# Optimization experiments

Measured on AMD Instinct MI355X. Metric: run time of the kernel, lower is better.

Reference implementation:

```python
import jax, jax.numpy as jnp
import numpy as np

NUM_EXPERTS = 8
PHM_DIM = 4


def setup_inputs() -> dict:
    key = jax.random.key(0)
    k1, k2, k3, k4 = jax.random.split(key, 4)
    bsz, seq, D, O, E, p = 4, 2048, 2048, 2048, NUM_EXPERTS, PHM_DIM
    hidden_states = jax.random.normal(k1, (bsz, seq, D), dtype=jnp.float32)
    gate_w = jax.random.normal(k2, (D, E), dtype=jnp.float32) * 0.02
    phm_rule = jax.random.normal(k3, (E, p, p, p), dtype=jnp.float32) * 0.1
    W = jax.random.normal(k4, (E, p, D // p, O // p), dtype=jnp.float32) * 0.02
    b = jnp.zeros((E, O), dtype=jnp.float32)
    return {"hidden_states": hidden_states, "gate_w": gate_w,
            "phm_rule": phm_rule, "W": W, "b": b}


def reference(hidden_states, gate_w, phm_rule, W, b):
    bsz, seq, dim = hidden_states.shape
    E = gate_w.shape[1]
    x = hidden_states.reshape(-1, dim)                      # [T, D]
    logits = x @ gate_w                                     # [T, E]
    prob = jax.nn.softmax(logits, axis=-1)                  # [T, E]
    gate = jnp.argmax(prob, axis=-1)                        # [T]
    # load-balancing loss
    num_tokens = jnp.sum(jax.nn.one_hot(gate, E, dtype=jnp.int32), axis=0)  # [E]
    f = num_tokens.astype(prob.dtype)
    f = f / jnp.sum(f)
    P = jnp.mean(prob, axis=0)
    balance_loss = E * jnp.sum(P * f)
    # PHM weight per expert: H_e = sum_p kron(phm_rule[e,p], W[e,p]) -> [E, D, O]
    Wfull = jnp.einsum('epab,epij->eaibj', phm_rule, W).reshape(E, dim, -1)
    # dense evaluation of every expert on every token, then top-1 select
    all_out = jnp.einsum('td,edo->teo', x, Wfull) + b[None, :, :]  # [T, E, O]
    tok_prob = jnp.take_along_axis(prob, gate[:, None], axis=1)    # [T, 1]
    out = jnp.take_along_axis(all_out, gate[:, None, None], axis=1)[:, 0, :] * tok_prob
    out = out.reshape(bsz, seq, -1)
    return out, balance_loss, num_tokens
```

## Files before the change

kernel.cpp:

```cpp
#include <hip/hip_runtime.h>
#include <cstdint>
#include <cstddef>

typedef _Float16 f16;
typedef f16 f16x2 __attribute__((ext_vector_type(2)));
typedef f16 f16x4 __attribute__((ext_vector_type(4)));
typedef f16 f16x8 __attribute__((ext_vector_type(8)));
typedef float f32x4 __attribute__((ext_vector_type(4)));

#define NEXP 8
#define BM 128
#define BN 128
#define BK 32

__device__ __forceinline__ void async_cp16(void* lds, const void* gsrc) {
  __builtin_amdgcn_global_load_lds(
      (const __attribute__((address_space(1))) void*)gsrc,
      (__attribute__((address_space(3))) void*)lds, 16, 0, 0);
}

__global__ __launch_bounds__(256) void k_gate(
    const float* __restrict__ x, const float* __restrict__ gw,
    f16* __restrict__ xb, int* __restrict__ gate, float* __restrict__ scale,
    int* __restrict__ cnt, float* __restrict__ probsum, int D)
{
  __shared__ float ps[NEXP];
  __shared__ int pc[NEXP];
  int tid = threadIdx.x, lane = tid & 63, w = tid >> 6;
  if (tid < NEXP) { ps[tid] = 0.f; pc[tid] = 0; }
  __syncthreads();

  int t = blockIdx.x * 4 + w;
  const float* xr = x + (size_t)t * D;
  f16* xbr = xb + (size_t)t * D;

  float acc[NEXP] = {};
  for (int d0 = lane * 4; d0 < D; d0 += 256) {
    float4 v = *(const float4*)(xr + d0);
    f16x4 h; h[0] = (f16)v.x; h[1] = (f16)v.y; h[2] = (f16)v.z; h[3] = (f16)v.w;
    *(f16x4*)(xbr + d0) = h;
    const float* g0 = gw + (size_t)d0 * NEXP;
    float xv[4] = {v.x, v.y, v.z, v.w};
#pragma unroll
    for (int j = 0; j < 4; j++) {
      float4 ga = *(const float4*)(g0 + j * NEXP);
      float4 gb = *(const float4*)(g0 + j * NEXP + 4);
      acc[0] += xv[j] * ga.x; acc[1] += xv[j] * ga.y;
      acc[2] += xv[j] * ga.z; acc[3] += xv[j] * ga.w;
      acc[4] += xv[j] * gb.x; acc[5] += xv[j] * gb.y;
      acc[6] += xv[j] * gb.z; acc[7] += xv[j] * gb.w;
    }
  }
#pragma unroll
  for (int e = 0; e < NEXP; e++) {
    float v = acc[e];
    for (int o = 32; o > 0; o >>= 1) v += __shfl_xor(v, o);
    acc[e] = v;
  }
  if (lane == 0) {
    float m = acc[0]; int g = 0;
#pragma unroll
    for (int e = 1; e < NEXP; e++) if (acc[e] > m) { m = acc[e]; g = e; }
    float pr[NEXP]; float ssum = 0.f;
#pragma unroll
    for (int e = 0; e < NEXP; e++) { pr[e] = expf(acc[e] - m); ssum += pr[e]; }
    float inv = 1.0f / ssum;
#pragma unroll
    for (int e = 0; e < NEXP; e++) atomicAdd(&ps[e], pr[e] * inv);
    atomicAdd(&pc[g], 1);
    gate[t] = g;
    scale[t] = pr[g] * inv;
  }
  __syncthreads();
  if (tid < NEXP) {
    atomicAdd(&probsum[tid], ps[tid]);
    atomicAdd(&cnt[tid], pc[tid]);
  }
}

__global__ __launch_bounds__(256) void k_wfull(
    const float* __restrict__ Wp, const float* __restrict__ rule,
    f16* __restrict__ wt, int Dp, int Op, int D, int O)
{
  int bid = blockIdx.x;
  int it = Dp >> 5, jt = Op >> 5;
  int itile = bid % it; bid /= it;
  int jtile = bid % jt; bid /= jt;
  int b = bid & 3; bid >>= 2;
  int e = bid;
  int i0 = itile * 32, j0 = jtile * 32;

  __shared__ float Wt[4][32][33];
  int tid = threadIdx.x;
  for (int idx = tid; idx < 4096; idx += 256) {
    int p = idx >> 10, rem = idx & 1023, ii = rem >> 5, jj = rem & 31;
    Wt[p][ii][jj] = Wp[(size_t)((e * 4 + p) * Dp + i0 + ii) * Op + j0 + jj];
  }
  float s[4][4];
#pragma unroll
  for (int p = 0; p < 4; p++)
#pragma unroll
    for (int a = 0; a < 4; a++)
      s[p][a] = rule[((e * 4 + p) * 4 + a) * 4 + b];
  __syncthreads();

  int ii = (tid & 15) * 2, jjb = tid >> 4;
#pragma unroll
  for (int a = 0; a < 4; a++) {
#pragma unroll
    for (int jp = 0; jp < 2; jp++) {
      int jj = jjb + jp * 16;
      float v0 = 0.f, v1 = 0.f;
#pragma unroll
      for (int p = 0; p < 4; p++) {
        v0 += s[p][a] * Wt[p][ii][jj];
        v1 += s[p][a] * Wt[p][ii + 1][jj];
      }
      size_t n = (size_t)b * Op + j0 + jj;
      size_t dd = (size_t)a * Dp + i0 + ii;
      f16x2 hv; hv[0] = (f16)v0; hv[1] = (f16)v1;
      *(f16x2*)(wt + ((size_t)e * O + n) * D + dd) = hv;
    }
  }
}

__global__ void k_plan(const int* __restrict__ cnt, const float* __restrict__ probsum,
                       int* __restrict__ offs, int* __restrict__ ndesc,
                       int2* __restrict__ desc, float* __restrict__ otail, int T)
{
  if (threadIdx.x != 0 || blockIdx.x != 0) return;
  int off = 0, nd = 0; float loss = 0.f;
  for (int e = 0; e < NEXP; e++) {
    offs[e] = off;
    int c = cnt[e];
    loss += probsum[e] * (float)c;
    for (int m0 = 0; m0 < c; m0 += BM) { desc[nd] = make_int2(e, m0); nd++; }
    off += c;
  }
  offs[NEXP] = off;
  *ndesc = nd;
  float invT = 1.0f / (float)T;
  otail[0] = (float)NEXP * loss * invT * invT;
  for (int e = 0; e < NEXP; e++) otail[1 + e] = (float)cnt[e];
}

__global__ __launch_bounds__(256) void k_scatter(
    const int* __restrict__ gate, const int* __restrict__ offs,
    int* __restrict__ cursor, int* __restrict__ perm)
{
  int t = blockIdx.x * 256 + threadIdx.x;
  int g = gate[t];
  int lane = threadIdx.x & 63;
  int pos = 0;
#pragma unroll
  for (int e = 0; e < NEXP; e++) {
    unsigned long long mask = __ballot(g == e);
    if (mask == 0ull) continue;
    int leader = __ffsll((unsigned long long)mask) - 1;
    int base = 0;
    if (lane == leader) base = atomicAdd(&cursor[e], (int)__popcll(mask));
    base = __shfl(base, leader);
    if (g == e) {
      int below = (int)__popcll(mask & ((1ull << lane) - 1ull));
      pos = offs[e] + base + below;
    }
  }
  perm[pos] = t;
}

__global__ __launch_bounds__(256) void k_gemm(
    const f16* __restrict__ xb, const f16* __restrict__ wt,
    const float* __restrict__ bias, const int* __restrict__ perm,
    const int* __restrict__ cnt, const int* __restrict__ offs,
    const int* __restrict__ ndesc, const int2* __restrict__ desc,
    const float* __restrict__ scale, float* __restrict__ out, int D, int O)
{
  if ((int)blockIdx.x >= *ndesc) return;
  int2 dsc = desc[blockIdx.x];
  int e = dsc.x, m0 = dsc.y;
  int ce = cnt[e];
  int seg = offs[e];
  int n0 = blockIdx.y * BN;

  __shared__ f16 Al[BM * BK];
  __shared__ f16 Bl[BN * BK];
  __shared__ int tokS[BM];
  __shared__ float scS[BM];

  int tid = threadIdx.x;
  if (tid < BM) {
    int idx = m0 + tid; if (idx > ce - 1) idx = ce - 1;
    int tok = perm[seg + idx];
    tokS[tid] = tok;
    scS[tid] = scale[tok];
  }
  __syncthreads();

  int r = tid >> 2;
  int c = tid & 3;
  const f16* a1 = xb + (size_t)tokS[r] * D + c * 8;
  const f16* a2 = xb + (size_t)tokS[r + 64] * D + c * 8;
  const f16* b1 = wt + ((size_t)e * O + n0 + r) * D + c * 8;
  const f16* b2 = wt + ((size_t)e * O + n0 + r + 64) * D + c * 8;
  f16* la1 = &Al[tid * 8];
  f16* la2 = &Al[2048 + tid * 8];
  f16* lb1 = &Bl[tid * 8];
  f16* lb2 = &Bl[2048 + tid * 8];

  int lane = tid & 63;
  int w = tid >> 6;
  int wm = (w & 1) * 64, wn = (w >> 1) * 64;
  int lr = lane & 15, q = lane >> 4;

  f32x4 acc[4][4] = {};

  int nk = D / BK;
  for (int kk = 0; kk < nk; ++kk) {
    async_cp16(la1, a1 + kk * BK);
    async_cp16(la2, a2 + kk * BK);
    async_cp16(lb1, b1 + kk * BK);
    async_cp16(lb2, b2 + kk * BK);
    __syncthreads();
    f16x8 af[4], bf[4];
#pragma unroll
    for (int mi = 0; mi < 4; mi++)
      af[mi] = *(const f16x8*)&Al[(wm + mi * 16 + lr) * BK + q * 8];
#pragma unroll
    for (int ni = 0; ni < 4; ni++)
      bf[ni] = *(const f16x8*)&Bl[(wn + ni * 16 + lr) * BK + q * 8];
#pragma unroll
    for (int mi = 0; mi < 4; mi++)
#pragma unroll
      for (int ni = 0; ni < 4; ni++)
        acc[mi][ni] = __builtin_amdgcn_mfma_f32_16x16x32_f16(
            af[mi], bf[ni], acc[mi][ni], 0, 0, 0);
    __syncthreads();
  }

  float bv[4];
#pragma unroll
  for (int ni = 0; ni < 4; ni++)
    bv[ni] = bias[(size_t)e * O + n0 + wn + ni * 16 + lr];
#pragma unroll
  for (int mi = 0; mi < 4; mi++) {
#pragma unroll
    for (int rg = 0; rg < 4; rg++) {
      int rl = wm + mi * 16 + q * 4 + rg;
      if (m0 + rl < ce) {
        float s = scS[rl];
        float* orow = out + (size_t)tokS[rl] * O + n0 + wn;
#pragma unroll
        for (int ni = 0; ni < 4; ni++)
          orow[ni * 16 + lr] = (acc[mi][ni][rg] + bv[ni]) * s;
      }
    }
  }
}

extern "C" void kernel_launch(void* const* d_in, const int* in_sizes, int n_in,
                              void* d_out, int out_size, void* d_ws, size_t ws_size,
                              hipStream_t stream)
{
  const float* x    = (const float*)d_in[0];
  const float* gw   = (const float*)d_in[1];
  const float* rule = (const float*)d_in[2];
  const float* W    = (const float*)d_in[3];
  const float* bias = (const float*)d_in[4];
  float* out = (float*)d_out;

  int D = in_sizes[1] / NEXP;
  int O = in_sizes[4] / NEXP;
  int T = in_sizes[0] / D;
  int Dp = D / 4, Op = O / 4;

  uint8_t* ws = (uint8_t*)d_ws;
  size_t off = 0;
  f16* xb = (f16*)(ws + off);  off += (size_t)T * D * 2;
  f16* wt = (f16*)(ws + off);  off += (size_t)NEXP * O * D * 2;
  int*   gate  = (int*)(ws + off);   off += (size_t)T * 4;
  float* scale = (float*)(ws + off); off += (size_t)T * 4;
  int*   perm  = (int*)(ws + off);   off += (size_t)T * 4;
  off = (off + 255) & ~(size_t)255;
  uint8_t* C = ws + off;
  int*   cnt     = (int*)(C + 0);
  float* probsum = (float*)(C + 32);
  int*   cursor  = (int*)(C + 64);
  int*   ndesc   = (int*)(C + 96);
  int*   offs    = (int*)(C + 128);
  int2*  desc    = (int2*)(C + 192);

  hipMemsetAsync(C, 0, 128, stream);

  k_gate<<<T / 4, 256, 0, stream>>>(x, gw, xb, gate, scale, cnt, probsum, D);
  k_wfull<<<NEXP * 4 * (Op / 32) * (Dp / 32), 256, 0, stream>>>(W, rule, wt, Dp, Op, D, O);
  k_plan<<<1, 1, 0, stream>>>(cnt, probsum, offs, ndesc, desc, out + (size_t)T * O, T);
  k_scatter<<<T / 256, 256, 0, stream>>>(gate, offs, cursor, perm);

  int maxdesc = T / BM + NEXP;
  k_gemm<<<dim3(maxdesc, O / BN), 256, 0, stream>>>(
      xb, wt, bias, perm, cnt, offs, ndesc, desc, scale, out, D, O);
}
```

Baseline: 382.8 us.

## Double-buffer GEMM LDS with swizzle and restructure gating kernel

The grouped GEMM now uses two LDS buffers and issues async global-to-LDS loads two k-steps ahead. It waits with explicit vmcnt and barriers, and the separate trailing sync is gone. An XOR swizzle on the 16-byte column chunks is meant to cut LDS bank conflicts on fragment reads. The gating kernel is rewritten to use a transposed gate weight produced by a new small kernel, with lanes split across experts and halves of D and softmax and argmax done via shuffles. The new hand-written waitcnt and barrier sequencing is fragile, and x is now read twice in the gating kernel.

```diff
diff --git a/kernel.cpp b/kernel.cpp
--- a/kernel.cpp
+++ b/kernel.cpp
@@ -19,62 +19,77 @@
       (__attribute__((address_space(3))) void*)lds, 16, 0, 0);
 }
 
-__global__ __launch_bounds__(256) void k_gate(
-    const float* __restrict__ x, const float* __restrict__ gw,
+__global__ __launch_bounds__(256) void k_gwT(const float* __restrict__ gw,
+                                             float* __restrict__ gwT, int D) {
+  int i = blockIdx.x * 256 + threadIdx.x;
+  int e = i / D, d = i - e * D;
+  gwT[i] = gw[d * NEXP + e];
+}
+
+__global__ __launch_bounds__(256) void k_gate2(
+    const float* __restrict__ x, const float* __restrict__ gwT,
     f16* __restrict__ xb, int* __restrict__ gate, float* __restrict__ scale,
     int* __restrict__ cnt, float* __restrict__ probsum, int D)
 {
-  __shared__ float ps[NEXP];
-  __shared__ int pc[NEXP];
-  int tid = threadIdx.x, lane = tid & 63, w = tid >> 6;
-  if (tid < NEXP) { ps[tid] = 0.f; pc[tid] = 0; }
+  __shared__ float lps[NEXP];
+  __shared__ int lcnt[NEXP];
+  int tid = threadIdx.x;
+  if (tid < NEXP) { lps[tid] = 0.f; lcnt[tid] = 0; }
   __syncthreads();
 
-  int t = blockIdx.x * 4 + w;
-  const float* xr = x + (size_t)t * D;
-  f16* xbr = xb + (size_t)t * D;
-
-  float acc[NEXP] = {};
-  for (int d0 = lane * 4; d0 < D; d0 += 256) {
-    float4 v = *(const float4*)(xr + d0);
-    f16x4 h; h[0] = (f16)v.x; h[1] = (f16)v.y; h[2] = (f16)v.z; h[3] = (f16)v.w;
-    *(f16x4*)(xbr + d0) = h;
-    const float* g0 = gw + (size_t)d0 * NEXP;
-    float xv[4] = {v.x, v.y, v.z, v.w};
-#pragma unroll
-    for (int j = 0; j < 4; j++) {
-      float4 ga = *(const float4*)(g0 + j * NEXP);
-      float4 gb = *(const float4*)(g0 + j * NEXP + 4);
-      acc[0] += xv[j] * ga.x; acc[1] += xv[j] * ga.y;
-      acc[2] += xv[j] * ga.z; acc[3] += xv[j] * ga.w;
-      acc[4] += xv[j] * gb.x; acc[5] += xv[j] * gb.y;
-      acc[6] += xv[j] * gb.z; acc[7] += xv[j] * gb.w;
-    }
-  }
-#pragma unroll
-  for (int e = 0; e < NEXP; e++) {
-    float v = acc[e];
-    for (int o = 32; o > 0; o >>= 1) v += __shfl_xor(v, o);
-    acc[e] = v;
-  }
-  if (lane == 0) {
-    float m = acc[0]; int g = 0;
-#pragma unroll
-    for (int e = 1; e < NEXP; e++) if (acc[e] > m) { m = acc[e]; g = e; }
-    float pr[NEXP]; float ssum = 0.f;
-#pragma unroll
-    for (int e = 0; e < NEXP; e++) { pr[e] = expf(acc[e] - m); ssum += pr[e]; }
-    float inv = 1.0f / ssum;
-#pragma unroll
-    for (int e = 0; e < NEXP; e++) atomicAdd(&ps[e], pr[e] * inv);
-    atomicAdd(&pc[g], 1);
-    gate[t] = g;
-    scale[t] = pr[g] * inv;
+  int t0 = blockIdx.x * 16;
+
+  for (int row = 0; row < 16; row++) {
+    const float* xr = x + (size_t)(t0 + row) * D;
+    f16* xo = xb + (size_t)(t0 + row) * D;
+    for (int cdx = tid * 4; cdx < D; cdx += 1024) {
+      float4 v = *(const float4*)(xr + cdx);
+      f16x4 h; h[0] = (f16)v.x; h[1] = (f16)v.y; h[2] = (f16)v.z; h[3] = (f16)v.w;
+      *(f16x4*)(xo + cdx) = h;
+    }
+  }
+
+  int lane = tid & 63, w = tid >> 6;
+  int dh = lane >> 5;
+  int tl = (lane >> 3) & 3;
+  int e  = lane & 7;
+  int tok = t0 + w * 4 + tl;
+  int halfD = D >> 1;
+  const float* xr = x + (size_t)tok * D + dh * halfD;
+  const float* gr = gwT + (size_t)e * D + dh * halfD;
+  float acc = 0.f;
+  for (int d = 0; d < halfD; d += 4) {
+    float4 xv = *(const float4*)(xr + d);
+    float4 gv = *(const float4*)(gr + d);
+    acc += xv.x * gv.x + xv.y * gv.y + xv.z * gv.z + xv.w * gv.w;
+  }
+  acc += __shfl_xor(acc, 32);
+
+  float v = acc;
+  float m = v;
+  m = fmaxf(m, __shfl_xor(m, 1));
+  m = fmaxf(m, __shfl_xor(m, 2));
+  m = fmaxf(m, __shfl_xor(m, 4));
+  float pe = __expf(v - m);
+  float s = pe;
+  s += __shfl_xor(s, 1); s += __shfl_xor(s, 2); s += __shfl_xor(s, 4);
+  int candv = (v == m) ? e : NEXP;
+  int g = candv;
+  g = min(g, __shfl_xor(g, 1)); g = min(g, __shfl_xor(g, 2)); g = min(g, __shfl_xor(g, 4));
+  float pg = __shfl(pe, (lane & 56) + g);
+
+  if (lane < 32) {
+    atomicAdd(&lps[e], pe / s);
+    if (e == 0) {
+      gate[tok] = g;
+      scale[tok] = pg / s;
+      atomicAdd(&lcnt[g], 1);
+    }
   }
   __syncthreads();
   if (tid < NEXP) {
-    atomicAdd(&probsum[tid], ps[tid]);
-    atomicAdd(&cnt[tid], pc[tid]);
+    atomicAdd(&probsum[tid], lps[tid]);
+    atomicAdd(&cnt[tid], lcnt[tid]);
   }
 }
 
@@ -182,8 +197,8 @@
   int seg = offs[e];
   int n0 = blockIdx.y * BN;
 
-  __shared__ f16 Al[BM * BK];
-  __shared__ f16 Bl[BN * BK];
+  __shared__ f16 Al[2][BM * BK];
+  __shared__ f16 Bl[2][BN * BK];
   __shared__ int tokS[BM];
   __shared__ float scS[BM];
 
@@ -198,44 +213,58 @@
 
   int r = tid >> 2;
   int c = tid & 3;
-  const f16* a1 = xb + (size_t)tokS[r] * D + c * 8;
-  const f16* a2 = xb + (size_t)tokS[r + 64] * D + c * 8;
-  const f16* b1 = wt + ((size_t)e * O + n0 + r) * D + c * 8;
-  const f16* b2 = wt + ((size_t)e * O + n0 + r + 64) * D + c * 8;
-  f16* la1 = &Al[tid * 8];
-  f16* la2 = &Al[2048 + tid * 8];
-  f16* lb1 = &Bl[tid * 8];
-  f16* lb2 = &Bl[2048 + tid * 8];
+  int gc = c ^ ((r >> 1) & 3);
+  const f16* a1 = xb + (size_t)tokS[r] * D + gc * 8;
+  const f16* a2 = xb + (size_t)tokS[r + 64] * D + gc * 8;
+  const f16* b1 = wt + ((size_t)e * O + n0 + r) * D + gc * 8;
+  const f16* b2 = wt + ((size_t)e * O + n0 + r + 64) * D + gc * 8;
 
   int lane = tid & 63;
   int w = tid >> 6;
   int wm = (w & 1) * 64, wn = (w >> 1) * 64;
   int lr = lane & 15, q = lane >> 4;
+  int qs = q ^ ((lr >> 1) & 3);
 
   f32x4 acc[4][4] = {};
-
   int nk = D / BK;
+
+#define STAGE(kk, p)                                             \
+  do {                                                           \
+    async_cp16(&Al[(p)][tid * 8], a1 + (kk) * BK);               \
+    async_cp16(&Al[(p)][2048 + tid * 8], a2 + (kk) * BK);        \
+    async_cp16(&Bl[(p)][tid * 8], b1 + (kk) * BK);               \
+    async_cp16(&Bl[(p)][2048 + tid * 8], b2 + (kk) * BK);        \
+  } while (0)
+
+  STAGE(0, 0);
+  STAGE(1, 1);
+
   for (int kk = 0; kk < nk; ++kk) {
-    async_cp16(la1, a1 + kk * BK);
-    async_cp16(la2, a2 + kk * BK);
-    async_cp16(lb1, b1 + kk * BK);
-    async_cp16(lb2, b2 + kk * BK);
-    __syncthreads();
+    int p = kk & 1;
+    if (kk + 1 < nk)
+      asm volatile("s_waitcnt vmcnt(4)\n\ts_barrier" ::: "memory");
+    else
+      asm volatile("s_waitcnt vmcnt(0)\n\ts_barrier" ::: "memory");
+
     f16x8 af[4], bf[4];
 #pragma unroll
     for (int mi = 0; mi < 4; mi++)
-      af[mi] = *(const f16x8*)&Al[(wm + mi * 16 + lr) * BK + q * 8];
+      af[mi] = *(const f16x8*)&Al[p][(wm + mi * 16 + lr) * BK + qs * 8];
 #pragma unroll
     for (int ni = 0; ni < 4; ni++)
-      bf[ni] = *(const f16x8*)&Bl[(wn + ni * 16 + lr) * BK + q * 8];
+      bf[ni] = *(const f16x8*)&Bl[p][(wn + ni * 16 + lr) * BK + qs * 8];
+
+    asm volatile("s_waitcnt lgkmcnt(0)\n\ts_barrier" ::: "memory");
+    if (kk + 2 < nk) STAGE(kk + 2, p);
+
 #pragma unroll
     for (int mi = 0; mi < 4; mi++)
 #pragma unroll
       for (int ni = 0; ni < 4; ni++)
         acc[mi][ni] = __builtin_amdgcn_mfma_f32_16x16x32_f16(
             af[mi], bf[ni], acc[mi][ni], 0, 0, 0);
-    __syncthreads();
-  }
+  }
+#undef STAGE
 
   float bv[4];
 #pragma unroll
@@ -288,10 +317,12 @@
   int*   ndesc   = (int*)(C + 96);
   int*   offs    = (int*)(C + 128);
   int2*  desc    = (int2*)(C + 192);
+  float* gwT     = (float*)(C + 4096);
 
   hipMemsetAsync(C, 0, 128, stream);
 
-  k_gate<<<T / 4, 256, 0, stream>>>(x, gw, xb, gate, scale, cnt, probsum, D);
+  k_gwT<<<(NEXP * D) / 256, 256, 0, stream>>>(gw, gwT, D);
+  k_gate2<<<T / 16, 256, 0, stream>>>(x, gwT, xb, gate, scale, cnt, probsum, D);
   k_wfull<<<NEXP * 4 * (Op / 32) * (Dp / 32), 256, 0, stream>>>(W, rule, wt, Dp, Op, D, O);
   k_plan<<<1, 1, 0, stream>>>(cnt, probsum, offs, ndesc, desc, out + (size_t)T * O, T);
   k_scatter<<<T / 256, 256, 0, stream>>>(gate, offs, cursor, perm);
```

After: 401.0 us. +4.7%, slower.
